# Kernel optimization log

Measured on AMD Instinct MI355X. Metric: run time of the kernel, lower is better.

The kernel has to match this reference:

```python
import jax, jax.numpy as jnp
import numpy as np

N, E = 10000, 320000
F_IN, HID, C_OUT = 256, 512, 128

def setup_inputs() -> dict:
    key = jax.random.key(0)
    ks = jax.random.split(key, 8)
    x = jax.random.normal(ks[0], (N, F_IN), dtype=jnp.float32)
    edge_index = jax.random.randint(ks[1], (2, E), 0, N, dtype=jnp.int64)
    s1 = 1.0 / np.sqrt(F_IN)
    s2 = 1.0 / np.sqrt(HID)
    # PyG SAGEConv: out = lin_l(aggr_sum(x_j)) + lin_r(x_i); lin_l has bias, lin_r does not
    W1l = jax.random.uniform(ks[2], (F_IN, HID), jnp.float32, -s1, s1)
    b1 = jnp.zeros((HID,), jnp.float32)
    W1r = jax.random.uniform(ks[3], (F_IN, HID), jnp.float32, -s1, s1)
    W2l = jax.random.uniform(ks[4], (HID, C_OUT), jnp.float32, -s2, s2)
    b2 = jnp.zeros((C_OUT,), jnp.float32)
    W2r = jax.random.uniform(ks[5], (HID, C_OUT), jnp.float32, -s2, s2)
    return {"x": x, "edge_index": edge_index, "W1l": W1l, "b1": b1,
            "W1r": W1r, "W2l": W2l, "b2": b2, "W2r": W2r}

def sage_conv(x, src, dst, Wl, b, Wr):
    # gather source-node features along edges, sum into target nodes, then linear
    agg = jax.ops.segment_sum(x[src], dst, num_segments=N)  # [N, F]
    return agg @ Wl + b + x @ Wr

def reference(x, edge_index, W1l, b1, W1r, W2l, b2, W2r):
    src, dst = edge_index[0], edge_index[1]
    h = sage_conv(x, src, dst, W1l, b1, W1r)
    h = jax.nn.relu(h)
    # F.dropout with training=False is identity (eval mode reference)
    out = sage_conv(h, src, dst, W2l, b2, W2r)
    return out
```

## Files before the change

kernel.cpp:

```cpp
#include <hip/hip_runtime.h>

#define N_NODES 10000
#define F_IN 256
#define HID 512
#define C_OUT 128
#define NEDGE 320000
#define BUCKET 128

typedef __attribute__((ext_vector_type(8))) short short8;
typedef __attribute__((ext_vector_type(4))) float floatx4;

__device__ inline float bf2f_lo(unsigned u) { union { float f; unsigned i; } v; v.i = u << 16; return v.f; }
__device__ inline float bf2f_hi(unsigned u) { union { float f; unsigned i; } v; v.i = u & 0xFFFF0000u; return v.f; }
__device__ inline unsigned short f2bf(float f) {
    union { float f; unsigned i; } v; v.f = f;
    unsigned r = (v.i + 0x7FFFu + ((v.i >> 16) & 1u)) >> 16;
    return (unsigned short)r;
}
__device__ inline void add8(float* a, uint4 v) {
    a[0] += bf2f_lo(v.x); a[1] += bf2f_hi(v.x);
    a[2] += bf2f_lo(v.y); a[3] += bf2f_hi(v.y);
    a[4] += bf2f_lo(v.z); a[5] += bf2f_hi(v.z);
    a[6] += bf2f_lo(v.w); a[7] += bf2f_hi(v.w);
}
__device__ inline int sel4(int4 v, int g) {
    return g == 0 ? v.x : (g == 1 ? v.y : (g == 2 ? v.z : v.w));
}

__device__ __forceinline__ void gload_lds16(const unsigned short* g, unsigned short* l) {
    __builtin_amdgcn_global_load_lds((const __attribute__((address_space(1))) void*)g,
                                     (__attribute__((address_space(3))) void*)l, 16, 0, 0);
}

__global__ __launch_bounds__(256)
void prep_kernel(const float4* __restrict__ xin, uint2* __restrict__ xb,
                 const float* __restrict__ W1l, const float* __restrict__ W1r,
                 const float* __restrict__ W2l, const float* __restrict__ W2r,
                 unsigned short* __restrict__ W1T, unsigned short* __restrict__ W2T,
                 int4* __restrict__ cursor4) {
    const int b = blockIdx.x;
    const int tid = threadIdx.x;
    if (b < 2500) {
        int i = b * 256 + tid;
        float4 v = xin[i];
        uint2 o;
        o.x = (unsigned)f2bf(v.x) | ((unsigned)f2bf(v.y) << 16);
        o.y = (unsigned)f2bf(v.z) | ((unsigned)f2bf(v.w) << 16);
        xb[i] = o;
        return;
    }
    if (b < 2884) {
        __shared__ float T[32][33];
        const int r = tid >> 3;
        const int c4 = (tid & 7) * 4;
        if (b < 2756) {
            int t = b - 2500;
            int kt = (t & 15) * 32, nt = (t >> 4) * 32;
            int kg = kt + r;
            const float* srcp = (kg < 256) ? (W1l + kg * 512) : (W1r + (kg - 256) * 512);
            float4 v = *(const float4*)(srcp + nt + c4);
            T[c4 + 0][r] = v.x; T[c4 + 1][r] = v.y; T[c4 + 2][r] = v.z; T[c4 + 3][r] = v.w;
            __syncthreads();
            ushort4 o;
            o.x = f2bf(T[r][c4 + 0]); o.y = f2bf(T[r][c4 + 1]);
            o.z = f2bf(T[r][c4 + 2]); o.w = f2bf(T[r][c4 + 3]);
            *(ushort4*)(W1T + (long long)(nt + r) * 512 + kt + c4) = o;
        } else {
            int t = b - 2756;
            int kt = (t & 15) * 32, col0 = (t >> 4) * 32;
            const float* Wsrc; int coloff;
            if (col0 < 128) { Wsrc = W2l; coloff = col0; } else { Wsrc = W2r; coloff = col0 - 128; }
            float4 v = *(const float4*)(Wsrc + (long long)(kt + r) * 128 + coloff + c4);
            T[c4 + 0][r] = v.x; T[c4 + 1][r] = v.y; T[c4 + 2][r] = v.z; T[c4 + 3][r] = v.w;
            __syncthreads();
            ushort4 o;
            o.x = f2bf(T[r][c4 + 0]); o.y = f2bf(T[r][c4 + 1]);
            o.z = f2bf(T[r][c4 + 2]); o.w = f2bf(T[r][c4 + 3]);
            *(ushort4*)(W2T + (long long)(col0 + r) * 512 + kt + c4) = o;
        }
        return;
    }
    {
        int i = (b - 2884) * 256 + tid;
        if (i < (N_NODES + 3) / 4) cursor4[i] = make_int4(0, 0, 0, 0);
    }
}

__global__ __launch_bounds__(256)
void fill_kernel(const int* __restrict__ src, const int* __restrict__ dst,
                 int* __restrict__ cursor, int* __restrict__ bucket, int E) {
    int e = blockIdx.x * 256 + threadIdx.x;
    if (e < E) {
        int d = dst[e];
        int pos = atomicAdd(&cursor[d], 1);
        bucket[(d << 7) + pos] = src[e];
    }
}

__global__ __launch_bounds__(256)
void gather_agg_256(const unsigned short* __restrict__ feat,
                    const int* __restrict__ cursor,
                    const int* __restrict__ bucket,
                    unsigned short* __restrict__ outp, int nnodes) {
    const int wid = (blockIdx.x * 256 + threadIdx.x) >> 6;
    if (wid >= nnodes) return;
    const int lane = threadIdx.x & 63;
    const int half = lane >> 5;
    const int sub = lane & 31;
    const long long myoff = (long long)sub * 8;
    const int cnt = __builtin_amdgcn_readfirstlane(cursor[wid]);
    const int* row = bucket + (wid << 7);

    float acc[8] = {0.f, 0.f, 0.f, 0.f, 0.f, 0.f, 0.f, 0.f};
    float accB[8] = {0.f, 0.f, 0.f, 0.f, 0.f, 0.f, 0.f, 0.f};

    int j = 0;
    for (; j + 16 <= cnt; j += 16) {
        const int4 ia = *(const int4*)(row + j);
        const int4 ib = *(const int4*)(row + j + 4);
        const int4 ic = *(const int4*)(row + j + 8);
        const int4 id = *(const int4*)(row + j + 12);
        int i0 = half ? ia.y : ia.x;
        int i1 = half ? ia.w : ia.z;
        int i2 = half ? ib.y : ib.x;
        int i3 = half ? ib.w : ib.z;
        int i4 = half ? ic.y : ic.x;
        int i5 = half ? ic.w : ic.z;
        int i6 = half ? id.y : id.x;
        int i7 = half ? id.w : id.z;
        uint4 v0 = *(const uint4*)(feat + (long long)i0 * 256 + myoff);
        uint4 v1 = *(const uint4*)(feat + (long long)i1 * 256 + myoff);
        uint4 v2 = *(const uint4*)(feat + (long long)i2 * 256 + myoff);
        uint4 v3 = *(const uint4*)(feat + (long long)i3 * 256 + myoff);
        uint4 v4 = *(const uint4*)(feat + (long long)i4 * 256 + myoff);
        uint4 v5 = *(const uint4*)(feat + (long long)i5 * 256 + myoff);
        uint4 v6 = *(const uint4*)(feat + (long long)i6 * 256 + myoff);
        uint4 v7 = *(const uint4*)(feat + (long long)i7 * 256 + myoff);
        add8(acc, v0); add8(accB, v1); add8(acc, v2); add8(accB, v3);
        add8(acc, v4); add8(accB, v5); add8(acc, v6); add8(accB, v7);
    }
    for (; j + 8 <= cnt; j += 8) {
        const int4 ia = *(const int4*)(row + j);
        const int4 ib = *(const int4*)(row + j + 4);
        int i0 = half ? ia.y : ia.x;
        int i1 = half ? ia.w : ia.z;
        int i2 = half ? ib.y : ib.x;
        int i3 = half ? ib.w : ib.z;
        uint4 v0 = *(const uint4*)(feat + (long long)i0 * 256 + myoff);
        uint4 v1 = *(const uint4*)(feat + (long long)i1 * 256 + myoff);
        uint4 v2 = *(const uint4*)(feat + (long long)i2 * 256 + myoff);
        uint4 v3 = *(const uint4*)(feat + (long long)i3 * 256 + myoff);
        add8(acc, v0); add8(accB, v1); add8(acc, v2); add8(accB, v3);
    }
    for (; j + 2 <= cnt; j += 2) {
        const int2 e = *(const int2*)(row + j);
        int i0 = half ? e.y : e.x;
        uint4 v = *(const uint4*)(feat + (long long)i0 * 256 + myoff);
        add8(acc, v);
    }
    if (j < cnt) {
        int i0 = row[j];
        uint4 v = *(const uint4*)(feat + (long long)i0 * 256 + myoff);
        if (half == 0) add8(acc, v);
    }
#pragma unroll
    for (int k = 0; k < 8; ++k) acc[k] += accB[k];
#pragma unroll
    for (int k = 0; k < 8; ++k) acc[k] += __shfl_xor(acc[k], 32, 64);

    if (half == 0) {
        uint4 o;
        o.x = (unsigned)f2bf(acc[0]) | ((unsigned)f2bf(acc[1]) << 16);
        o.y = (unsigned)f2bf(acc[2]) | ((unsigned)f2bf(acc[3]) << 16);
        o.z = (unsigned)f2bf(acc[4]) | ((unsigned)f2bf(acc[5]) << 16);
        o.w = (unsigned)f2bf(acc[6]) | ((unsigned)f2bf(acc[7]) << 16);
        *(uint4*)(outp + (long long)wid * 256 + myoff) = o;
    }
}

__global__ __launch_bounds__(256)
void gather_acc_128(const unsigned short* __restrict__ feat,
                    const int* __restrict__ cursor,
                    const int* __restrict__ bucket,
                    float* __restrict__ outp, int nnodes) {
    const int wid = (blockIdx.x * 256 + threadIdx.x) >> 6;
    if (wid >= nnodes) return;
    const int lane = threadIdx.x & 63;
    const int g = lane >> 4;
    const int sub = lane & 15;
    const long long myoff = (long long)sub * 8;
    const int cnt = __builtin_amdgcn_readfirstlane(cursor[wid]);
    const int* row = bucket + (wid << 7);

    float4 c0 = make_float4(0.f, 0.f, 0.f, 0.f), c1 = c0;
    float* orow = outp + (long long)wid * 128 + sub * 8;
    if (lane < 16) {
        c0 = *(const float4*)(orow);
        c1 = *(const float4*)(orow + 4);
    }

    float acc[8] = {0.f, 0.f, 0.f, 0.f, 0.f, 0.f, 0.f, 0.f};
    float accB[8] = {0.f, 0.f, 0.f, 0.f, 0.f, 0.f, 0.f, 0.f};

    int j = 0;
    for (; j + 16 <= cnt; j += 16) {
        const int4 ia = *(const int4*)(row + j);
        const int4 ib = *(const int4*)(row + j + 4);
        const int4 ic = *(const int4*)(row + j + 8);
        const int4 id = *(const int4*)(row + j + 12);
        int i0 = sel4(ia, g), i1 = sel4(ib, g), i2 = sel4(ic, g), i3 = sel4(id, g);
        uint4 v0 = *(const uint4*)(feat + (long long)i0 * 128 + myoff);
        uint4 v1 = *(const uint4*)(feat + (long long)i1 * 128 + myoff);
        uint4 v2 = *(const uint4*)(feat + (long long)i2 * 128 + myoff);
        uint4 v3 = *(const uint4*)(feat + (long long)i3 * 128 + myoff);
        add8(acc, v0); add8(accB, v1); add8(acc, v2); add8(accB, v3);
    }
    for (; j + 8 <= cnt; j += 8) {
        const int4 ia = *(const int4*)(row + j);
        const int4 ib = *(const int4*)(row + j + 4);
        int i0 = sel4(ia, g), i1 = sel4(ib, g);
        uint4 v0 = *(const uint4*)(feat + (long long)i0 * 128 + myoff);
        uint4 v1 = *(const uint4*)(feat + (long long)i1 * 128 + myoff);
        add8(acc, v0); add8(accB, v1);
    }
    for (; j + 4 <= cnt; j += 4) {
        const int4 ia = *(const int4*)(row + j);
        int i0 = sel4(ia, g);
        uint4 v = *(const uint4*)(feat + (long long)i0 * 128 + myoff);
        add8(acc, v);
    }
    int rem = cnt - j;
    if (rem > 0) {
        int idx = row[j + (g < rem ? g : 0)];
        uint4 v = *(const uint4*)(feat + (long long)idx * 128 + myoff);
        if (g < rem) add8(acc, v);
    }
#pragma unroll
    for (int k = 0; k < 8; ++k) acc[k] += accB[k];
#pragma unroll
    for (int k = 0; k < 8; ++k) acc[k] += __shfl_xor(acc[k], 16, 64);
#pragma unroll
    for (int k = 0; k < 8; ++k) acc[k] += __shfl_xor(acc[k], 32, 64);

    if (lane < 16) {
        c0.x += acc[0]; c0.y += acc[1]; c0.z += acc[2]; c0.w += acc[3];
        c1.x += acc[4]; c1.y += acc[5]; c1.z += acc[6]; c1.w += acc[7];
        *(float4*)(orow) = c0;
        *(float4*)(orow + 4) = c1;
    }
}

template <int MODE>
__global__ __launch_bounds__(256)
void mfma_gemm(const unsigned short* __restrict__ A1, int K1,
               const unsigned short* __restrict__ A2, int K2,
               const unsigned short* __restrict__ BT,
               const float* __restrict__ bias,
               void* __restrict__ C0v, void* __restrict__ C1v,
               int M, int Nfull) {
    __shared__ unsigned short A_lds[128][64];
    __shared__ unsigned short B_lds[64][64];

    const int t = threadIdx.x;
    const int lane = t & 63;
    const int w = t >> 6;
    const int l15 = lane & 15;
    const int quad = lane >> 4;
    const int row0 = blockIdx.x * 128;
    const int col0 = blockIdx.y * 64;
    const int Ktot = K1 + K2;

    floatx4 acc[2][4];
#pragma unroll
    for (int i = 0; i < 2; ++i)
#pragma unroll
        for (int cf = 0; cf < 4; ++cf) acc[i][cf] = (floatx4){0.f, 0.f, 0.f, 0.f};

    const int lr = lane >> 3;
    const int gchunk = (lane & 7) ^ lr;

    for (int k0 = 0; k0 < Ktot; k0 += 64) {
        const unsigned short* Ap;
        int astride, acol;
        if (k0 < K1) { Ap = A1; astride = K1; acol = k0; }
        else         { Ap = A2; astride = K2; acol = k0 - K1; }
#pragma unroll
        for (int it = 0; it < 4; ++it) {
            int r = w * 32 + it * 8 + lr;
            int gr = row0 + r; if (gr >= M) gr = M - 1;
            gload_lds16(Ap + (long long)gr * astride + acol + gchunk * 8,
                        &A_lds[w * 32 + it * 8][0]);
        }
#pragma unroll
        for (int it = 0; it < 2; ++it) {
            int r = w * 16 + it * 8 + lr;
            gload_lds16(BT + (long long)(col0 + r) * Ktot + k0 + gchunk * 8,
                        &B_lds[w * 16 + it * 8][0]);
        }
        __syncthreads();
#pragma unroll
        for (int kc = 0; kc < 2; ++kc) {
            const int sa = ((kc * 4 + quad) ^ (l15 & 7)) * 8;
            short8 a0 = *(short8*)&A_lds[w * 32 + l15][sa];
            short8 a1 = *(short8*)&A_lds[w * 32 + 16 + l15][sa];
            short8 bb[4];
#pragma unroll
            for (int cf = 0; cf < 4; ++cf)
                bb[cf] = *(short8*)&B_lds[cf * 16 + l15][sa];
#pragma unroll
            for (int cf = 0; cf < 4; ++cf) {
                acc[0][cf] = __builtin_amdgcn_mfma_f32_16x16x32_bf16(a0, bb[cf], acc[0][cf], 0, 0, 0);
                acc[1][cf] = __builtin_amdgcn_mfma_f32_16x16x32_bf16(a1, bb[cf], acc[1][cf], 0, 0, 0);
            }
        }
        __syncthreads();
    }

    const int rbase = row0 + w * 32 + quad * 4;

    if (MODE == 0) {
        unsigned short* C0 = (unsigned short*)C0v;
#pragma unroll
        for (int cf = 0; cf < 4; ++cf) {
            const int cj = col0 + cf * 16 + l15;
            const float bi = bias[cj];
#pragma unroll
            for (int i = 0; i < 2; ++i) {
#pragma unroll
                for (int reg = 0; reg < 4; ++reg) {
                    int r = rbase + i * 16 + reg;
                    if (r >= M) continue;
                    C0[(long long)r * Nfull + cj] = f2bf(fmaxf(acc[i][cf][reg] + bi, 0.f));
                }
            }
        }
    } else {
        if (col0 < 128) {
            unsigned short* C0 = (unsigned short*)C0v;
#pragma unroll
            for (int cf = 0; cf < 4; ++cf) {
                const int cj = col0 + cf * 16 + l15;
#pragma unroll
                for (int i = 0; i < 2; ++i) {
#pragma unroll
                    for (int reg = 0; reg < 4; ++reg) {
                        int r = rbase + i * 16 + reg;
                        if (r >= M) continue;
                        C0[(long long)r * 128 + cj] = f2bf(acc[i][cf][reg]);
                    }
                }
            }
        } else {
            float* C1 = (float*)C1v;
#pragma unroll
            for (int cf = 0; cf < 4; ++cf) {
                const int d = col0 - 128 + cf * 16 + l15;
                const float bi = bias[d];
#pragma unroll
                for (int i = 0; i < 2; ++i) {
#pragma unroll
                    for (int reg = 0; reg < 4; ++reg) {
                        int r = rbase + i * 16 + reg;
                        if (r >= M) continue;
                        C1[(long long)r * 128 + d] = acc[i][cf][reg] + bi;
                    }
                }
            }
        }
    }
}

extern "C" void kernel_launch(void* const* d_in, const int* in_sizes, int n_in,
                              void* d_out, int out_size, void* d_ws, size_t ws_size,
                              hipStream_t stream) {
    const float* x   = (const float*)d_in[0];
    const int*   ei  = (const int*)d_in[1];
    const float* W1l = (const float*)d_in[2];
    const float* b1  = (const float*)d_in[3];
    const float* W1r = (const float*)d_in[4];
    const float* W2l = (const float*)d_in[5];
    const float* b2  = (const float*)d_in[6];
    const float* W2r = (const float*)d_in[7];
    float* out = (float*)d_out;

    const int E = in_sizes[1] / 2;
    const int* src = ei;
    const int* dst = ei + E;

    char* w = (char*)d_ws;
    int* cursor  = (int*)w;             w += 10016 * sizeof(int);
    int* bucket  = (int*)w;             w += (long long)N_NODES * BUCKET * sizeof(int);
    unsigned short* xb    = (unsigned short*)w; w += (long long)N_NODES * F_IN * 2;
    unsigned short* agg1b = (unsigned short*)w; w += (long long)N_NODES * F_IN * 2;
    unsigned short* W1T   = (unsigned short*)w; w += 512 * 512 * 2;
    unsigned short* W2T   = (unsigned short*)w; w += 256 * 512 * 2;
    unsigned short* h     = (unsigned short*)w; w += (long long)N_NODES * HID * 2;
    unsigned short* p     = (unsigned short*)w; w += (long long)N_NODES * C_OUT * 2;

    prep_kernel<<<2894, 256, 0, stream>>>((const float4*)x, (uint2*)xb,
                                          W1l, W1r, W2l, W2r, W1T, W2T, (int4*)cursor);
    fill_kernel<<<(E + 255) / 256, 256, 0, stream>>>(src, dst, cursor, bucket, E);

    const int agg_blocks = (N_NODES * 64 + 255) / 256;

    gather_agg_256<<<agg_blocks, 256, 0, stream>>>(xb, cursor, bucket, agg1b, N_NODES);
    {
        dim3 grid((N_NODES + 127) / 128, HID / 64);
        mfma_gemm<0><<<grid, 256, 0, stream>>>(agg1b, F_IN, xb, F_IN, W1T, b1,
                                               (void*)h, (void*)nullptr, N_NODES, HID);
    }

    {
        dim3 grid((N_NODES + 127) / 128, 256 / 64);
        mfma_gemm<1><<<grid, 256, 0, stream>>>(h, HID, h, 0, W2T, b2,
                                               (void*)p, (void*)out, N_NODES, 256);
    }
    gather_acc_128<<<agg_blocks, 256, 0, stream>>>(p, cursor, bucket, out, N_NODES);
}
```

Measured before the change: 162.0 us.

## Split layer-1 gather into two half-feature passes with four edge groups per wave

The 256-wide layer-1 neighbor aggregation is split into two launches, each covering 128 feature columns. Each wave now splits into four 16-lane groups that handle four edges at once instead of two, and the groups are combined with two xor shuffles. The aim is to shrink the per-pass gather working set so it fits better in cache and to get more edges in flight per wave. The cost is a second launch and reading the bucket indices twice.

```diff
diff --git a/kernel.cpp b/kernel.cpp
--- a/kernel.cpp
+++ b/kernel.cpp
@@ -98,15 +98,15 @@
 }
 
 __global__ __launch_bounds__(256)
-void gather_agg_256(const unsigned short* __restrict__ feat,
-                    const int* __restrict__ cursor,
-                    const int* __restrict__ bucket,
-                    unsigned short* __restrict__ outp, int nnodes) {
+void gather_agg_half(const unsigned short* __restrict__ feat,
+                     const int* __restrict__ cursor,
+                     const int* __restrict__ bucket,
+                     unsigned short* __restrict__ outp, int nnodes) {
     const int wid = (blockIdx.x * 256 + threadIdx.x) >> 6;
     if (wid >= nnodes) return;
     const int lane = threadIdx.x & 63;
-    const int half = lane >> 5;
-    const int sub = lane & 31;
+    const int g = lane >> 4;
+    const int sub = lane & 15;
     const long long myoff = (long long)sub * 8;
     const int cnt = __builtin_amdgcn_readfirstlane(cursor[wid]);
     const int* row = bucket + (wid << 7);
@@ -120,55 +120,41 @@
         const int4 ib = *(const int4*)(row + j + 4);
         const int4 ic = *(const int4*)(row + j + 8);
         const int4 id = *(const int4*)(row + j + 12);
-        int i0 = half ? ia.y : ia.x;
-        int i1 = half ? ia.w : ia.z;
-        int i2 = half ? ib.y : ib.x;
-        int i3 = half ? ib.w : ib.z;
-        int i4 = half ? ic.y : ic.x;
-        int i5 = half ? ic.w : ic.z;
-        int i6 = half ? id.y : id.x;
-        int i7 = half ? id.w : id.z;
-        uint4 v0 = *(const uint4*)(feat + (long long)i0 * 256 + myoff);
-        uint4 v1 = *(const uint4*)(feat + (long long)i1 * 256 + myoff);
-        uint4 v2 = *(const uint4*)(feat + (long long)i2 * 256 + myoff);
-        uint4 v3 = *(const uint4*)(feat + (long long)i3 * 256 + myoff);
-        uint4 v4 = *(const uint4*)(feat + (long long)i4 * 256 + myoff);
-        uint4 v5 = *(const uint4*)(feat + (long long)i5 * 256 + myoff);
-        uint4 v6 = *(const uint4*)(feat + (long long)i6 * 256 + myoff);
-        uint4 v7 = *(const uint4*)(feat + (long long)i7 * 256 + myoff);
-        add8(acc, v0); add8(accB, v1); add8(acc, v2); add8(accB, v3);
-        add8(acc, v4); add8(accB, v5); add8(acc, v6); add8(accB, v7);
-    }
-    for (; j + 8 <= cnt; j += 8) {
-        const int4 ia = *(const int4*)(row + j);
-        const int4 ib = *(const int4*)(row + j + 4);
-        int i0 = half ? ia.y : ia.x;
-        int i1 = half ? ia.w : ia.z;
-        int i2 = half ? ib.y : ib.x;
-        int i3 = half ? ib.w : ib.z;
+        int i0 = sel4(ia, g), i1 = sel4(ib, g), i2 = sel4(ic, g), i3 = sel4(id, g);
         uint4 v0 = *(const uint4*)(feat + (long long)i0 * 256 + myoff);
         uint4 v1 = *(const uint4*)(feat + (long long)i1 * 256 + myoff);
         uint4 v2 = *(const uint4*)(feat + (long long)i2 * 256 + myoff);
         uint4 v3 = *(const uint4*)(feat + (long long)i3 * 256 + myoff);
         add8(acc, v0); add8(accB, v1); add8(acc, v2); add8(accB, v3);
     }
-    for (; j + 2 <= cnt; j += 2) {
-        const int2 e = *(const int2*)(row + j);
-        int i0 = half ? e.y : e.x;
+    for (; j + 8 <= cnt; j += 8) {
+        const int4 ia = *(const int4*)(row + j);
+        const int4 ib = *(const int4*)(row + j + 4);
+        int i0 = sel4(ia, g), i1 = sel4(ib, g);
+        uint4 v0 = *(const uint4*)(feat + (long long)i0 * 256 + myoff);
+        uint4 v1 = *(const uint4*)(feat + (long long)i1 * 256 + myoff);
+        add8(acc, v0); add8(accB, v1);
+    }
+    for (; j + 4 <= cnt; j += 4) {
+        const int4 ia = *(const int4*)(row + j);
+        int i0 = sel4(ia, g);
         uint4 v = *(const uint4*)(feat + (long long)i0 * 256 + myoff);
         add8(acc, v);
     }
-    if (j < cnt) {
-        int i0 = row[j];
-        uint4 v = *(const uint4*)(feat + (long long)i0 * 256 + myoff);
-        if (half == 0) add8(acc, v);
+    int rem = cnt - j;
+    if (rem > 0) {
+        int idx = row[j + (g < rem ? g : 0)];
+        uint4 v = *(const uint4*)(feat + (long long)idx * 256 + myoff);
+        if (g < rem) add8(acc, v);
     }
 #pragma unroll
     for (int k = 0; k < 8; ++k) acc[k] += accB[k];
 #pragma unroll
+    for (int k = 0; k < 8; ++k) acc[k] += __shfl_xor(acc[k], 16, 64);
+#pragma unroll
     for (int k = 0; k < 8; ++k) acc[k] += __shfl_xor(acc[k], 32, 64);
 
-    if (half == 0) {
+    if (lane < 16) {
         uint4 o;
         o.x = (unsigned)f2bf(acc[0]) | ((unsigned)f2bf(acc[1]) << 16);
         o.y = (unsigned)f2bf(acc[2]) | ((unsigned)f2bf(acc[3]) << 16);
@@ -403,7 +389,8 @@
 
     const int agg_blocks = (N_NODES * 64 + 255) / 256;
 
-    gather_agg_256<<<agg_blocks, 256, 0, stream>>>(xb, cursor, bucket, agg1b, N_NODES);
+    gather_agg_half<<<agg_blocks, 256, 0, stream>>>(xb,       cursor, bucket, agg1b,       N_NODES);
+    gather_agg_half<<<agg_blocks, 256, 0, stream>>>(xb + 128, cursor, bucket, agg1b + 128, N_NODES);
     {
         dim3 grid((N_NODES + 127) / 128, HID / 64);
         mfma_gemm<0><<<grid, 256, 0, stream>>>(agg1b, F_IN, xb, F_IN, W1T, b1,
```

Result: slower. 167.8 us (+3.6%).
